# Optimization experiments

Hardware: AMD Instinct MI355X
Metric: run time of the kernel (lower is better)

Reference implementation:

```python
import jax, jax.numpy as jnp
import numpy as np

N_NODES = 10000
N_EDGES = 640000
D_IN = 128
D_OUT = 128


def setup_inputs() -> dict:
    key = jax.random.key(0)
    k_x, k_val, k_w, k_row, k_col = jax.random.split(key, 5)
    # Glorot init for weight, zeros for bias (matches _weight_init)
    limit = float(np.sqrt(6.0 / (D_IN + D_OUT)))
    weight = jax.random.uniform(k_w, (D_IN, D_OUT), jnp.float32, -limit, limit)
    return {
        "x": jax.random.normal(k_x, (N_NODES, D_IN), jnp.float32),
        "adj_val": jax.random.uniform(k_val, (N_EDGES,), jnp.float32),  # normalized edge weights of sparse adj
        "weight": weight,
        "bias": jnp.zeros((D_OUT,), jnp.float32),
        "adj_row": jax.random.randint(k_row, (N_EDGES,), 0, N_NODES, jnp.int32),
        "adj_col": jax.random.randint(k_col, (N_EDGES,), 0, N_NODES, jnp.int32),
    }


def reference(x, adj_val, weight, bias, adj_row, adj_col):
    # dense GEMM: h = x @ W  -> [N, D_OUT]
    h = jnp.matmul(x, weight)
    # SpMM with COO adjacency: out[r] = sum_{e: row[e]=r} val[e] * h[col[e]]
    msg = adj_val[:, None] * h[adj_col]  # [E, D_OUT] gather + scale
    out = jax.ops.segment_sum(msg, adj_row, num_segments=x.shape[0])
    return out + bias
```

## Files before the change

kernel.cpp:

```cpp
#include <hip/hip_runtime.h>

#define N_NODES 10000
#define N_EDGES 640000
#define D 128

#define GEMM_BLOCKS 157
#define TOT_BLOCKS 256
#define CAP 32
#define OVF_CAP 8192
#define LSTR 136
#define QPAD 272

typedef unsigned int uint32;
typedef unsigned short u16;
using short8 = __attribute__((ext_vector_type(8))) short;
using f32x4  = __attribute__((ext_vector_type(4))) float;

__device__ __forceinline__ uint32 f2bf_bits(float f) {
    uint32 u = __float_as_uint(f);
    return (u + 0x7FFFu + ((u >> 16) & 1u)) >> 16;
}
__device__ __forceinline__ uint32 pack2(float lo, float hi) {
    return f2bf_bits(lo) | (f2bf_bits(hi) << 16);
}

__device__ __forceinline__ void scat_one(int r, uint32 rc, int s,
                                         int* __restrict__ cursor,
                                         uint32* __restrict__ region,
                                         int* ovf_cnt, uint2* ovf)
{
    int pos = atomicAdd(&cursor[s * N_NODES + r], 1);
    if (pos < CAP) {
        region[(r * 8 + s) * CAP + pos] = rc;
    } else {
        int o = atomicAdd(ovf_cnt, 1);
        if (o < OVF_CAP) ovf[o] = make_uint2((uint32)r, rc);
    }
}

__global__ __launch_bounds__(256) void gemm_scatter_kernel(
    const float* __restrict__ x, const float* __restrict__ w,
    const int* __restrict__ row, const int* __restrict__ col,
    const float* __restrict__ val,
    uint32* __restrict__ h2, int* __restrict__ cursor,
    int* __restrict__ ovf_cnt, uint2* __restrict__ ovf,
    uint32* __restrict__ region)
{
    const int t = threadIdx.x;

    if (blockIdx.x < GEMM_BLOCKS) {
        __shared__ u16 Xs[64 * LSTR];
        __shared__ u16 Ws[128 * LSTR];

        #pragma unroll
        for (int i = 0; i < 8; ++i) {
            int lin = t + i * 256;
            int rw  = lin >> 5;
            int f4  = lin & 31;
            int gr = blockIdx.x * 64 + rw;
            if (gr >= N_NODES) gr = N_NODES - 1;
            float4 xv = *(const float4*)&x[(size_t)gr * D + f4 * 4];
            *(uint2*)&Xs[rw * LSTR + f4 * 4] =
                make_uint2(pack2(xv.x, xv.y), pack2(xv.z, xv.w));
        }
        #pragma unroll
        for (int i = 0; i < 32; ++i) {
            int lin = t + i * 256;
            int c = lin & 127;
            int m = lin >> 7;
            float w0 = w[(2 * m) * D + c];
            float w1 = w[(2 * m + 1) * D + c];
            *(uint32*)&Ws[c * LSTR + 2 * m] = pack2(w0, w1);
        }
        __syncthreads();

        const int wv = t >> 6, lane = t & 63;
        const int q = lane >> 4, cl = lane & 15;
        f32x4 acc[8] = {};
        const u16* arow = &Xs[(wv * 16 + cl) * LSTR];
        #pragma unroll
        for (int k0 = 0; k0 < D; k0 += 32) {
            short8 af = *(const short8*)&arow[k0 + q * 8];
            #pragma unroll
            for (int ct = 0; ct < 8; ++ct) {
                short8 bf = *(const short8*)&Ws[(ct * 16 + cl) * LSTR + k0 + q * 8];
                acc[ct] = __builtin_amdgcn_mfma_f32_16x16x32_bf16(af, bf, acc[ct], 0, 0, 0);
            }
        }
        #pragma unroll
        for (int reg = 0; reg < 4; ++reg) {
            int node = blockIdx.x * 64 + wv * 16 + q * 4 + reg;
            if (node < N_NODES) {
                uint32* base = h2 + (size_t)node * 64 + cl;
                #pragma unroll
                for (int ct = 0; ct < 4; ++ct)
                    base[ct * 16] = pack2(acc[ct][reg], acc[ct + 4][reg]);
            }
        }
    }

    {
        const int xcc = blockIdx.x & 7;
        const int tid    = blockIdx.x * 256 + t;
        const int stride = TOT_BLOCKS * 256;
        const int4*   row4 = (const int4*)row;
        const int4*   col4 = (const int4*)col;
        const float4* val4 = (const float4*)val;
        for (int i = tid; i < N_EDGES / 4; i += stride) {
            int4 r = row4[i]; int4 c = col4[i]; float4 v = val4[i];
            scat_one(r.x, (uint32)c.x | (f2bf_bits(v.x) << 16), xcc, cursor, region, ovf_cnt, ovf);
            scat_one(r.y, (uint32)c.y | (f2bf_bits(v.y) << 16), xcc, cursor, region, ovf_cnt, ovf);
            scat_one(r.z, (uint32)c.z | (f2bf_bits(v.z) << 16), xcc, cursor, region, ovf_cnt, ovf);
            scat_one(r.w, (uint32)c.w | (f2bf_bits(v.w) << 16), xcc, cursor, region, ovf_cnt, ovf);
        }
    }
}

__global__ __launch_bounds__(256) void spmm_kernel(
    const uint32* __restrict__ region, const int* __restrict__ cursor,
    const int* __restrict__ ovf_cnt, const uint2* __restrict__ ovf,
    const uint32* __restrict__ h2, const float* __restrict__ bias,
    float* __restrict__ out)
{
    __shared__ uint32 qbuf[4 * QPAD];
    const int t = threadIdx.x;
    const int lane = t & 63;
    const int wid  = t >> 6;
    const int r = blockIdx.x * 4 + wid;
    uint32* qb = &qbuf[wid * QPAD];

    uint32 rl[4];
    #pragma unroll
    for (int i = 0; i < 4; ++i)
        rl[i] = region[r * 256 + i * 64 + lane];

    int ns[8], pref[9];
    pref[0] = 0;
    #pragma unroll
    for (int s = 0; s < 8; ++s) {
        int c = cursor[s * N_NODES + r];
        ns[s] = (c < CAP) ? c : CAP;
        pref[s + 1] = pref[s] + ns[s];
    }
    const int ntot = pref[8];

    #pragma unroll
    for (int i = 0; i < 4; ++i) {
        int p  = lane & 31;
        int hi = lane >> 5;
        int n_  = hi ? ns[2 * i + 1]   : ns[2 * i];
        int pf  = hi ? pref[2 * i + 1] : pref[2 * i];
        if (p < n_) qb[pf + p] = rl[i];
    }
    if (lane < 16) qb[ntot + lane] = 0;
    __builtin_amdgcn_s_waitcnt(0);

    const int npad = (ntot + 7) & ~7;
    float a0 = 0.f, a1 = 0.f;

    uint32 rq0,rq1,rq2,rq3,rq4,rq5,rq6,rq7;
    uint32 hh0,hh1,hh2,hh3,hh4,hh5,hh6,hh7;
    rq0 = qb[0]; hh0 = h2[((rq0 & 0xFFFFu) << 6) + lane];
    rq1 = qb[1]; hh1 = h2[((rq1 & 0xFFFFu) << 6) + lane];
    rq2 = qb[2]; hh2 = h2[((rq2 & 0xFFFFu) << 6) + lane];
    rq3 = qb[3]; hh3 = h2[((rq3 & 0xFFFFu) << 6) + lane];
    rq4 = qb[4]; hh4 = h2[((rq4 & 0xFFFFu) << 6) + lane];
    rq5 = qb[5]; hh5 = h2[((rq5 & 0xFFFFu) << 6) + lane];
    rq6 = qb[6]; hh6 = h2[((rq6 & 0xFFFFu) << 6) + lane];
    rq7 = qb[7]; hh7 = h2[((rq7 & 0xFFFFu) << 6) + lane];

#define CONSUME_PREFETCH(RQ, HH, P)                                          \
    {                                                                        \
        a0 = fmaf(__uint_as_float(RQ & 0xFFFF0000u),                         \
                  __uint_as_float(HH << 16), a0);                            \
        a1 = fmaf(__uint_as_float(RQ & 0xFFFF0000u),                         \
                  __uint_as_float(HH & 0xFFFF0000u), a1);                    \
        uint32 rn = qb[j + 8 + P];                                           \
        RQ = rn; HH = h2[((rn & 0xFFFFu) << 6) + lane];                      \
    }

    for (int j = 0; j < npad; j += 8) {
        CONSUME_PREFETCH(rq0, hh0, 0)
        CONSUME_PREFETCH(rq1, hh1, 1)
        CONSUME_PREFETCH(rq2, hh2, 2)
        CONSUME_PREFETCH(rq3, hh3, 3)
        CONSUME_PREFETCH(rq4, hh4, 4)
        CONSUME_PREFETCH(rq5, hh5, 5)
        CONSUME_PREFETCH(rq6, hh6, 6)
        CONSUME_PREFETCH(rq7, hh7, 7)
    }
#undef CONSUME_PREFETCH

    int novf = ovf_cnt[0];
    if (novf > OVF_CAP) novf = OVF_CAP;
    for (int k = 0; k < novf; ++k) {
        uint2 e = ovf[k];
        if (e.x == (uint32)r) {
            uint32 qq = e.y;
            uint32 hv = h2[((qq & 0xFFFFu) << 6) + lane];
            a0 = fmaf(__uint_as_float(qq & 0xFFFF0000u), __uint_as_float(hv << 16), a0);
            a1 = fmaf(__uint_as_float(qq & 0xFFFF0000u), __uint_as_float(hv & 0xFFFF0000u), a1);
        }
    }

    out[(size_t)r * D + lane]      = a0 + bias[lane];
    out[(size_t)r * D + 64 + lane] = a1 + bias[lane + 64];
}

extern "C" void kernel_launch(void* const* d_in, const int* in_sizes, int n_in,
                              void* d_out, int out_size, void* d_ws, size_t ws_size,
                              hipStream_t stream)
{
    const float* x    = (const float*)d_in[0];
    const float* aval = (const float*)d_in[1];
    const float* w    = (const float*)d_in[2];
    const float* bias = (const float*)d_in[3];
    const int* arow   = (const int*)d_in[4];
    const int* acol   = (const int*)d_in[5];

    char* ws = (char*)d_ws;
    uint32* h2     = (uint32*)(ws);
    int*    cursor = (int*)(ws + 2560000);
    int*    ovfcnt = (int*)(ws + 2880000);
    uint2*  ovf    = (uint2*)(ws + 2880064);
    uint32* region = (uint32*)(ws + 2945600);

    hipMemsetAsync(ws + 2560000, 0, 320004, stream);

    gemm_scatter_kernel<<<TOT_BLOCKS, 256, 0, stream>>>(
        x, w, arow, acol, aval, h2, cursor, ovfcnt, ovf, region);
    spmm_kernel<<<N_NODES / 4, 256, 0, stream>>>(
        region, cursor, ovfcnt, ovf, h2, bias, (float*)d_out);
}
```

Before: 115.0 us.

## Fuse memset, GEMM-scatter and SpMM into one cooperative persistent kernel

Replaces the memset plus two kernel launches with a single cooperative kernel of 512 blocks that zeroes the cursors, runs the GEMM and the edge scatter, then does the SpMM in a grid-stride loop over rows, with grid-wide barriers between phases. The goal is to remove launch overhead and the gaps between kernels. The scatter phase also gets twice as many blocks. In exchange it adds two grid.sync barriers and shared memory for all phases in every block, and it needs two blocks per CU to be resident, which may limit occupancy for the SpMM gather.

```diff
diff --git a/kernel.cpp b/kernel.cpp
--- a/kernel.cpp
+++ b/kernel.cpp
@@ -1,11 +1,14 @@
 #include <hip/hip_runtime.h>
+#include <hip/hip_cooperative_groups.h>
+
+namespace cg = cooperative_groups;
 
 #define N_NODES 10000
 #define N_EDGES 640000
 #define D 128
 
+#define BLOCKS 512
 #define GEMM_BLOCKS 157
-#define TOT_BLOCKS 256
 #define CAP 32
 #define OVF_CAP 8192
 #define LSTR 136
@@ -38,26 +41,36 @@
     }
 }
 
-__global__ __launch_bounds__(256) void gemm_scatter_kernel(
+__global__ void __launch_bounds__(256, 2) fused_kernel(
     const float* __restrict__ x, const float* __restrict__ w,
     const int* __restrict__ row, const int* __restrict__ col,
-    const float* __restrict__ val,
+    const float* __restrict__ val, const float* __restrict__ bias,
     uint32* __restrict__ h2, int* __restrict__ cursor,
     int* __restrict__ ovf_cnt, uint2* __restrict__ ovf,
-    uint32* __restrict__ region)
+    uint32* __restrict__ region, float* __restrict__ out)
 {
+    __shared__ u16 Xs[64 * LSTR];
+    __shared__ u16 Ws[128 * LSTR];
+    __shared__ uint32 qbuf[4 * QPAD];
+
+    cg::grid_group grid = cg::this_grid();
     const int t = threadIdx.x;
-
-    if (blockIdx.x < GEMM_BLOCKS) {
-        __shared__ u16 Xs[64 * LSTR];
-        __shared__ u16 Ws[128 * LSTR];
-
+    const int b = blockIdx.x;
+
+    {
+        int idx = b * 256 + t;
+        if (idx < 8 * N_NODES) cursor[idx] = 0;
+        else if (idx == 8 * N_NODES) *ovf_cnt = 0;
+    }
+    grid.sync();
+
+    if (b < GEMM_BLOCKS) {
         #pragma unroll
         for (int i = 0; i < 8; ++i) {
             int lin = t + i * 256;
             int rw  = lin >> 5;
             int f4  = lin & 31;
-            int gr = blockIdx.x * 64 + rw;
+            int gr = b * 64 + rw;
             if (gr >= N_NODES) gr = N_NODES - 1;
             float4 xv = *(const float4*)&x[(size_t)gr * D + f4 * 4];
             *(uint2*)&Xs[rw * LSTR + f4 * 4] =
@@ -89,7 +102,7 @@
         }
         #pragma unroll
         for (int reg = 0; reg < 4; ++reg) {
-            int node = blockIdx.x * 64 + wv * 16 + q * 4 + reg;
+            int node = b * 64 + wv * 16 + q * 4 + reg;
             if (node < N_NODES) {
                 uint32* base = h2 + (size_t)node * 64 + cl;
                 #pragma unroll
@@ -100,9 +113,9 @@
     }
 
     {
-        const int xcc = blockIdx.x & 7;
-        const int tid    = blockIdx.x * 256 + t;
-        const int stride = TOT_BLOCKS * 256;
+        const int xcc = b & 7;
+        const int tid    = b * 256 + t;
+        const int stride = BLOCKS * 256;
         const int4*   row4 = (const int4*)row;
         const int4*   col4 = (const int4*)col;
         const float4* val4 = (const float4*)val;
@@ -114,97 +127,95 @@
             scat_one(r.w, (uint32)c.w | (f2bf_bits(v.w) << 16), xcc, cursor, region, ovf_cnt, ovf);
         }
     }
-}
-
-__global__ __launch_bounds__(256) void spmm_kernel(
-    const uint32* __restrict__ region, const int* __restrict__ cursor,
-    const int* __restrict__ ovf_cnt, const uint2* __restrict__ ovf,
-    const uint32* __restrict__ h2, const float* __restrict__ bias,
-    float* __restrict__ out)
-{
-    __shared__ uint32 qbuf[4 * QPAD];
-    const int t = threadIdx.x;
-    const int lane = t & 63;
-    const int wid  = t >> 6;
-    const int r = blockIdx.x * 4 + wid;
-    uint32* qb = &qbuf[wid * QPAD];
-
-    uint32 rl[4];
-    #pragma unroll
-    for (int i = 0; i < 4; ++i)
-        rl[i] = region[r * 256 + i * 64 + lane];
-
-    int ns[8], pref[9];
-    pref[0] = 0;
-    #pragma unroll
-    for (int s = 0; s < 8; ++s) {
-        int c = cursor[s * N_NODES + r];
-        ns[s] = (c < CAP) ? c : CAP;
-        pref[s + 1] = pref[s] + ns[s];
-    }
-    const int ntot = pref[8];
-
-    #pragma unroll
-    for (int i = 0; i < 4; ++i) {
-        int p  = lane & 31;
-        int hi = lane >> 5;
-        int n_  = hi ? ns[2 * i + 1]   : ns[2 * i];
-        int pf  = hi ? pref[2 * i + 1] : pref[2 * i];
-        if (p < n_) qb[pf + p] = rl[i];
-    }
-    if (lane < 16) qb[ntot + lane] = 0;
-    __builtin_amdgcn_s_waitcnt(0);
-
-    const int npad = (ntot + 7) & ~7;
-    float a0 = 0.f, a1 = 0.f;
-
-    uint32 rq0,rq1,rq2,rq3,rq4,rq5,rq6,rq7;
-    uint32 hh0,hh1,hh2,hh3,hh4,hh5,hh6,hh7;
-    rq0 = qb[0]; hh0 = h2[((rq0 & 0xFFFFu) << 6) + lane];
-    rq1 = qb[1]; hh1 = h2[((rq1 & 0xFFFFu) << 6) + lane];
-    rq2 = qb[2]; hh2 = h2[((rq2 & 0xFFFFu) << 6) + lane];
-    rq3 = qb[3]; hh3 = h2[((rq3 & 0xFFFFu) << 6) + lane];
-    rq4 = qb[4]; hh4 = h2[((rq4 & 0xFFFFu) << 6) + lane];
-    rq5 = qb[5]; hh5 = h2[((rq5 & 0xFFFFu) << 6) + lane];
-    rq6 = qb[6]; hh6 = h2[((rq6 & 0xFFFFu) << 6) + lane];
-    rq7 = qb[7]; hh7 = h2[((rq7 & 0xFFFFu) << 6) + lane];
+    grid.sync();
+
+    {
+        const int lane = t & 63;
+        const int wid  = t >> 6;
+        uint32* qb = &qbuf[wid * QPAD];
+        const float bb0 = bias[lane];
+        const float bb1 = bias[lane + 64];
+        const int gw = b * 4 + wid;
+        const int novf0 = ovf_cnt[0];
+        const int novf = (novf0 > OVF_CAP) ? OVF_CAP : novf0;
+
+        for (int r = gw; r < N_NODES; r += BLOCKS * 4) {
+            uint32 rl[4];
+            #pragma unroll
+            for (int i = 0; i < 4; ++i)
+                rl[i] = region[r * 256 + i * 64 + lane];
+
+            int ns[8], pref[9];
+            pref[0] = 0;
+            #pragma unroll
+            for (int s = 0; s < 8; ++s) {
+                int c = cursor[s * N_NODES + r];
+                ns[s] = (c < CAP) ? c : CAP;
+                pref[s + 1] = pref[s] + ns[s];
+            }
+            const int ntot = pref[8];
+
+            #pragma unroll
+            for (int i = 0; i < 4; ++i) {
+                int p  = lane & 31;
+                int hi = lane >> 5;
+                int n_  = hi ? ns[2 * i + 1]   : ns[2 * i];
+                int pf  = hi ? pref[2 * i + 1] : pref[2 * i];
+                if (p < n_) qb[pf + p] = rl[i];
+            }
+            if (lane < 16) qb[ntot + lane] = 0;
+            __builtin_amdgcn_s_waitcnt(0);
+
+            const int npad = (ntot + 7) & ~7;
+            float a0 = 0.f, a1 = 0.f;
+
+            uint32 rq0,rq1,rq2,rq3,rq4,rq5,rq6,rq7;
+            uint32 hh0,hh1,hh2,hh3,hh4,hh5,hh6,hh7;
+            rq0 = qb[0]; hh0 = h2[((rq0 & 0xFFFFu) << 6) + lane];
+            rq1 = qb[1]; hh1 = h2[((rq1 & 0xFFFFu) << 6) + lane];
+            rq2 = qb[2]; hh2 = h2[((rq2 & 0xFFFFu) << 6) + lane];
+            rq3 = qb[3]; hh3 = h2[((rq3 & 0xFFFFu) << 6) + lane];
+            rq4 = qb[4]; hh4 = h2[((rq4 & 0xFFFFu) << 6) + lane];
+            rq5 = qb[5]; hh5 = h2[((rq5 & 0xFFFFu) << 6) + lane];
+            rq6 = qb[6]; hh6 = h2[((rq6 & 0xFFFFu) << 6) + lane];
+            rq7 = qb[7]; hh7 = h2[((rq7 & 0xFFFFu) << 6) + lane];
 
 #define CONSUME_PREFETCH(RQ, HH, P)                                          \
-    {                                                                        \
-        a0 = fmaf(__uint_as_float(RQ & 0xFFFF0000u),                         \
-                  __uint_as_float(HH << 16), a0);                            \
-        a1 = fmaf(__uint_as_float(RQ & 0xFFFF0000u),                         \
-                  __uint_as_float(HH & 0xFFFF0000u), a1);                    \
-        uint32 rn = qb[j + 8 + P];                                           \
-        RQ = rn; HH = h2[((rn & 0xFFFFu) << 6) + lane];                      \
-    }
-
-    for (int j = 0; j < npad; j += 8) {
-        CONSUME_PREFETCH(rq0, hh0, 0)
-        CONSUME_PREFETCH(rq1, hh1, 1)
-        CONSUME_PREFETCH(rq2, hh2, 2)
-        CONSUME_PREFETCH(rq3, hh3, 3)
-        CONSUME_PREFETCH(rq4, hh4, 4)
-        CONSUME_PREFETCH(rq5, hh5, 5)
-        CONSUME_PREFETCH(rq6, hh6, 6)
-        CONSUME_PREFETCH(rq7, hh7, 7)
-    }
+            {                                                                \
+                a0 = fmaf(__uint_as_float(RQ & 0xFFFF0000u),                 \
+                          __uint_as_float(HH << 16), a0);                    \
+                a1 = fmaf(__uint_as_float(RQ & 0xFFFF0000u),                 \
+                          __uint_as_float(HH & 0xFFFF0000u), a1);            \
+                uint32 rn = qb[j + 8 + P];                                   \
+                RQ = rn; HH = h2[((rn & 0xFFFFu) << 6) + lane];              \
+            }
+
+            for (int j = 0; j < npad; j += 8) {
+                CONSUME_PREFETCH(rq0, hh0, 0)
+                CONSUME_PREFETCH(rq1, hh1, 1)
+                CONSUME_PREFETCH(rq2, hh2, 2)
+                CONSUME_PREFETCH(rq3, hh3, 3)
+                CONSUME_PREFETCH(rq4, hh4, 4)
+                CONSUME_PREFETCH(rq5, hh5, 5)
+                CONSUME_PREFETCH(rq6, hh6, 6)
+                CONSUME_PREFETCH(rq7, hh7, 7)
+            }
 #undef CONSUME_PREFETCH
 
-    int novf = ovf_cnt[0];
-    if (novf > OVF_CAP) novf = OVF_CAP;
-    for (int k = 0; k < novf; ++k) {
-        uint2 e = ovf[k];
-        if (e.x == (uint32)r) {
-            uint32 qq = e.y;
-            uint32 hv = h2[((qq & 0xFFFFu) << 6) + lane];
-            a0 = fmaf(__uint_as_float(qq & 0xFFFF0000u), __uint_as_float(hv << 16), a0);
-            a1 = fmaf(__uint_as_float(qq & 0xFFFF0000u), __uint_as_float(hv & 0xFFFF0000u), a1);
-        }
-    }
-
-    out[(size_t)r * D + lane]      = a0 + bias[lane];
-    out[(size_t)r * D + 64 + lane] = a1 + bias[lane + 64];
+            for (int k = 0; k < novf; ++k) {
+                uint2 e = ovf[k];
+                if (e.x == (uint32)r) {
+                    uint32 qq = e.y;
+                    uint32 hv = h2[((qq & 0xFFFFu) << 6) + lane];
+                    a0 = fmaf(__uint_as_float(qq & 0xFFFF0000u), __uint_as_float(hv << 16), a0);
+                    a1 = fmaf(__uint_as_float(qq & 0xFFFF0000u), __uint_as_float(hv & 0xFFFF0000u), a1);
+                }
+            }
+
+            out[(size_t)r * D + lane]      = a0 + bb0;
+            out[(size_t)r * D + 64 + lane] = a1 + bb1;
+        }
+    }
 }
 
 extern "C" void kernel_launch(void* const* d_in, const int* in_sizes, int n_in,
@@ -224,11 +235,11 @@
     int*    ovfcnt = (int*)(ws + 2880000);
     uint2*  ovf    = (uint2*)(ws + 2880064);
     uint32* region = (uint32*)(ws + 2945600);
-
-    hipMemsetAsync(ws + 2560000, 0, 320004, stream);
-
-    gemm_scatter_kernel<<<TOT_BLOCKS, 256, 0, stream>>>(
-        x, w, arow, acol, aval, h2, cursor, ovfcnt, ovf, region);
-    spmm_kernel<<<N_NODES / 4, 256, 0, stream>>>(
-        region, cursor, ovfcnt, ovf, h2, bias, (float*)d_out);
-}
+    float*  out    = (float*)d_out;
+
+    void* args[] = { (void*)&x, (void*)&w, (void*)&arow, (void*)&acol,
+                     (void*)&aval, (void*)&bias, (void*)&h2, (void*)&cursor,
+                     (void*)&ovfcnt, (void*)&ovf, (void*)&region, (void*)&out };
+    hipLaunchCooperativeKernel((void*)fused_kernel, dim3(BLOCKS), dim3(256),
+                               args, 0, stream);
+}
```

Result: slower. 245.5 us (+113.4%).
